# Kernel optimization log

Hardware: AMD Instinct MI355X
Metric: run time of the kernel (lower is better)

Reference implementation:

```python
import jax, jax.numpy as jnp
import numpy as np

ROUTINGS = 3


def squash(v):
    # squash along last axis: v/|v| * |v|^2/(1+|v|^2)
    norm = jnp.linalg.norm(v, axis=-1, keepdims=True)
    ns = norm * norm
    return v / norm * (ns / (1.0 + ns))


def setup_inputs() -> dict:
    key = jax.random.key(0)
    k1, k2 = jax.random.split(key)
    B, N, I, D, Din = 256, 10, 1152, 16, 8
    inputs = jax.random.normal(k1, (B, I, Din), dtype=jnp.float32)
    # glorot-uniform-ish init for W [N, I, D, Din]
    limit = np.sqrt(6.0 / (D + Din)).astype(np.float32)
    W = jax.random.uniform(k2, (N, I, D, Din), dtype=jnp.float32,
                           minval=-limit, maxval=limit)
    return {"inputs": inputs, "W": W}


def reference(inputs, W):
    # inputs: [B, I, Din], W: [N, I, D, Din]
    # u_hat[b,n,i,d] = sum_k W[n,i,d,k] * inputs[b,i,k]  (replaces tf.map_fn)
    u_hat = jnp.einsum('nidk,bik->bnid', W, inputs)  # [B, N, I, D]
    b = jnp.zeros(u_hat.shape[:3], dtype=u_hat.dtype)  # [B, N, I]
    outputs = None
    for r in range(ROUTINGS):
        c = jax.nn.softmax(b, axis=1)  # softmax over output capsules N
        outputs = squash(jnp.einsum('bni,bnid->bnd', c, u_hat))  # [B, N, D]
        if r < ROUTINGS - 1:
            # agreement: a[b,n,i] = <outputs[b,n,:], u_hat[b,n,i,:]>
            b = b + jnp.einsum('bnd,bnid->bni', outputs, u_hat)
    return outputs
```

## Files before the change

### kernel.cpp

```cpp
#include <hip/hip_runtime.h>
#include <hip/hip_bf16.h>
#include <stdint.h>


#define BN 256
#define NN 10
#define II 1152
#define DD 16
#define KK 8
#define NT 18
#define NCH 6
#define CHI 192

typedef unsigned short ushort_t;
typedef unsigned int uint_t;

__device__ __forceinline__ float bflo(uint_t u) {
    union { uint_t i; float f; } v; v.i = u << 16; return v.f;
}
__device__ __forceinline__ float bfhi(uint_t u) {
    union { uint_t i; float f; } v; v.i = u & 0xffff0000u; return v.f;
}
__device__ __forceinline__ uint_t pkbf(float lo, float hi) {
    __hip_bfloat162 h = __float22bfloat162_rn(make_float2(lo, hi));
    uint_t u; __builtin_memcpy(&u, &h, sizeof(u)); return u;
}

__global__ __launch_bounds__(256) void caps_uhat_s0(const float* __restrict__ xg,
                                                    const float* __restrict__ wg,
                                                    ushort_t* __restrict__ u,
                                                    float* __restrict__ part0,
                                                    int b0, int c4)
{
    __shared__ float red[16][NN][16];
    const int tid = threadIdx.x;
    const int lane = tid & 63, wv = tid >> 6;
    const int dq = lane & 3, il = lane >> 2;
    const int nb8 = gridDim.x >> 3;
    const int L   = (blockIdx.x & 7) * nb8 + (blockIdx.x >> 3);
    const int it  = L / c4;
    const int bl  = (L - it * c4) * 4;
    const int i = it * 64 + wv * 16 + il;

    float xv[4][8];
#pragma unroll
    for (int bb = 0; bb < 4; ++bb) {
        const float4* xp = (const float4*)(xg + ((size_t)(b0 + bl + bb) * II + i) * KK);
        float4 x0 = xp[0], x1 = xp[1];
        xv[bb][0] = x0.x; xv[bb][1] = x0.y; xv[bb][2] = x0.z; xv[bb][3] = x0.w;
        xv[bb][4] = x1.x; xv[bb][5] = x1.y; xv[bb][6] = x1.z; xv[bb][7] = x1.w;
    }

    for (int n = 0; n < NN; ++n) {
        const float4* wp = (const float4*)(wg + (size_t)(n * II + i) * (DD * KK)) + dq * 8;
        float4 w[8];
#pragma unroll
        for (int j = 0; j < 8; ++j) w[j] = wp[j];

        float s[4][4];
#pragma unroll
        for (int dj = 0; dj < 4; ++dj) {
            float4 wa = w[2 * dj], wb = w[2 * dj + 1];
#pragma unroll
            for (int bb = 0; bb < 4; ++bb) {
                s[bb][dj] = wa.x * xv[bb][0] + wa.y * xv[bb][1]
                          + wa.z * xv[bb][2] + wa.w * xv[bb][3]
                          + wb.x * xv[bb][4] + wb.y * xv[bb][5]
                          + wb.z * xv[bb][6] + wb.w * xv[bb][7];
            }
        }
#pragma unroll
        for (int bb = 0; bb < 4; ++bb) {
            uint2 q;
            q.x = pkbf(s[bb][0], s[bb][1]);
            q.y = pkbf(s[bb][2], s[bb][3]);
            *(uint2*)(u + (((size_t)(bl + bb) * NN + n) * II + i) * DD + dq * 4) = q;
        }
#pragma unroll
        for (int m = 4; m <= 32; m <<= 1)
#pragma unroll
            for (int bb = 0; bb < 4; ++bb)
#pragma unroll
                for (int dj = 0; dj < 4; ++dj)
                    s[bb][dj] += __shfl_xor(s[bb][dj], m, 64);
        if (il == 0) {
#pragma unroll
            for (int bb = 0; bb < 4; ++bb)
#pragma unroll
                for (int dj = 0; dj < 4; ++dj)
                    red[wv * 4 + dq][n][bb * 4 + dj] = s[bb][dj];
        }
    }
    __syncthreads();
#pragma unroll
    for (int idx = tid; idx < 640; idx += 256) {
        int bb = idx / 160, r = idx - bb * 160;
        int n = r >> 4, d = r & 15, q2 = d >> 2, dj = d & 3;
        float v = red[0 + q2][n][bb * 4 + dj] + red[4 + q2][n][bb * 4 + dj]
                + red[8 + q2][n][bb * 4 + dj] + red[12 + q2][n][bb * 4 + dj];
        part0[((size_t)(b0 + bl + bb) * NT + it) * 160 + r] = 0.1f * v;
    }
}

__device__ __forceinline__ void block_reduce_part(float sp[NN][4], int tid,
                                                  float* red,
                                                  float* __restrict__ partp)
{
#pragma unroll
    for (int m = 4; m <= 32; m <<= 1)
#pragma unroll
        for (int n = 0; n < NN; ++n)
#pragma unroll
            for (int j = 0; j < 4; ++j)
                sp[n][j] += __shfl_xor(sp[n][j], m, 64);

    const int lane = tid & 63, wv = tid >> 6, ld = tid & 3;
    if (lane < 4) {
#pragma unroll
        for (int n = 0; n < NN; ++n)
#pragma unroll
            for (int j = 0; j < 4; ++j)
                red[(wv * NN + n) * 16 + ld * 4 + j] = sp[n][j];
    }
    __syncthreads();
    if (tid < 160) {
        int n = tid >> 4, dd = tid & 15;
        float v = 0.f;
#pragma unroll
        for (int w = 0; w < 4; ++w) v += red[(w * NN + n) * 16 + dd];
        partp[tid] = v;
    }
}

__global__ __launch_bounds__(256) void caps_sweep(const ushort_t* __restrict__ u,
                                                  const float* __restrict__ p0,
                                                  const float* __restrict__ p1,
                                                  float* __restrict__ pout, int b0)
{
    __shared__ float red[4 * 160];
    __shared__ float o_s[160];
    const int tid = threadIdx.x, g = tid >> 2, ld = tid & 3;
    const int cb = blockIdx.x / NCH, ch = blockIdx.x % NCH;
    const int b = b0 + cb;
    const ushort_t* ub = u + (size_t)cb * (NN * II * DD);

    if (tid < 160) {
        float v = 0.f;
#pragma unroll
        for (int t = 0; t < NT; ++t)
            v += p0[((size_t)b * NT + t) * 160 + tid];
        float sq = v * v;
#pragma unroll
        for (int m = 1; m <= 8; m <<= 1) sq += __shfl_xor(sq, m, 64);
        float o = v * (sqrtf(sq) / (1.0f + sq));
        if (p1) {
            float v1 = 0.f;
#pragma unroll
            for (int c2 = 0; c2 < NCH; ++c2)
                v1 += p1[((size_t)b * NCH + c2) * 160 + tid];
            float sq1 = v1 * v1;
#pragma unroll
            for (int m = 1; m <= 8; m <<= 1) sq1 += __shfl_xor(sq1, m, 64);
            o += v1 * (sqrtf(sq1) / (1.0f + sq1));
        }
        o_s[tid] = o;
    }
    __syncthreads();

    float sp[NN][4];
#pragma unroll
    for (int n = 0; n < NN; ++n)
#pragma unroll
        for (int j = 0; j < 4; ++j) sp[n][j] = 0.f;

    const int i0 = ch * CHI + g;
    uint2 r[NN];
#pragma unroll
    for (int n = 0; n < NN; ++n)
        r[n] = *(const uint2*)(ub + ((size_t)(n * II + i0)) * DD + ld * 4);

#pragma unroll
    for (int step = 0; step < CHI / 64; ++step) {
        uint2 rn[NN];
        if (step + 1 < CHI / 64) {
            const int i2 = i0 + (step + 1) * 64;
#pragma unroll
            for (int n = 0; n < NN; ++n)
                rn[n] = *(const uint2*)(ub + ((size_t)(n * II + i2)) * DD + ld * 4);
        }

        float p[NN];
#pragma unroll
        for (int n = 0; n < NN; ++n) {
            float4 o4 = *(const float4*)&o_s[(n << 4) + (ld << 2)];
            p[n] = bflo(r[n].x) * o4.x + bfhi(r[n].x) * o4.y
                 + bflo(r[n].y) * o4.z + bfhi(r[n].y) * o4.w;
        }
        float a[NN];
#pragma unroll
        for (int n = 0; n < NN; ++n) {
            float t2 = p[n] + __shfl_xor(p[n], 1, 64);
            a[n] = t2 + __shfl_xor(t2, 2, 64);
        }
        float m = a[0];
#pragma unroll
        for (int n = 1; n < NN; ++n) m = fmaxf(m, a[n]);
        float c[NN], ssum = 0.f;
#pragma unroll
        for (int n = 0; n < NN; ++n) { c[n] = __expf(a[n] - m); ssum += c[n]; }
        float inv = 1.0f / ssum;
#pragma unroll
        for (int n = 0; n < NN; ++n) {
            float w = c[n] * inv;
            sp[n][0] += w * bflo(r[n].x); sp[n][1] += w * bfhi(r[n].x);
            sp[n][2] += w * bflo(r[n].y); sp[n][3] += w * bfhi(r[n].y);
        }
        if (step + 1 < CHI / 64) {
#pragma unroll
            for (int n = 0; n < NN; ++n) r[n] = rn[n];
        }
    }
    block_reduce_part(sp, tid, red, pout + ((size_t)b * NCH + ch) * 160);
}

__global__ __launch_bounds__(192) void caps_out(const float* __restrict__ p2,
                                                float* __restrict__ out, int b0)
{
    const int b = b0 + blockIdx.x;
    const int t = threadIdx.x;
    if (t < 160) {
        float v = 0.f;
#pragma unroll
        for (int ch = 0; ch < NCH; ++ch)
            v += p2[((size_t)b * NCH + ch) * 160 + t];
        float sq = v * v;
#pragma unroll
        for (int m = 1; m <= 8; m <<= 1) sq += __shfl_xor(sq, m, 64);
        out[(size_t)b * 160 + t] = v * (sqrtf(sq) / (1.0f + sq));
    }
}

extern "C" void kernel_launch(void* const* d_in, const int* in_sizes, int n_in,
                              void* d_out, int out_size, void* d_ws, size_t ws_size,
                              hipStream_t stream)
{
    const float* xg = (const float*)d_in[0];
    const float* wg = (const float*)d_in[1];
    if (n_in >= 2 && in_sizes[0] == NN * II * DD * KK) {
        const float* t = xg; xg = wg; wg = t;
    }
    float* outp = (float*)d_out;

    const size_t perB  = (size_t)NN * II * DD * 2;
    const size_t p0B   = (size_t)BN * NT * 160 * 4;
    const size_t p12B  = (size_t)BN * NCH * 160 * 4;
    size_t extra = p0B + 2 * p12B;
    size_t avail = (ws_size > extra) ? ws_size - extra : 0;
    int C = 256;
    if (avail < (size_t)256 * perB) {
        C = (int)(avail / perB);
        C &= ~15;
        if (C < 16) C = 16;
    }
    ushort_t* uws = (ushort_t*)d_ws;
    float* part0 = (float*)((char*)d_ws + (size_t)C * perB);
    float* part1 = part0 + (size_t)BN * NT * 160;
    float* part2 = part1 + (size_t)BN * NCH * 160;

    for (int b0 = 0; b0 < BN; b0 += C) {
        int c = (BN - b0 < C) ? (BN - b0) : C;
        int c4 = c / 4;
        caps_uhat_s0<<<NT * c4, 256, 0, stream>>>(xg, wg, uws, part0, b0, c4);
        caps_sweep  <<<c * NCH, 256, 0, stream>>>(uws, part0, nullptr, part1, b0);
        caps_sweep  <<<c * NCH, 256, 0, stream>>>(uws, part0, part1,  part2, b0);
        caps_out    <<<c,       192, 0, stream>>>(part2, outp, b0);
    }
}
```

Measured before the change: 168.6 us.

## Use butterfly reduce-scatter in u_hat kernel, halve routing chunks, drop prefetch

The u_hat kernel's 16-value cross-lane sum is replaced with a recursive-halving reduce-scatter. Each shuffle stage now exchanges only half the values, so each lane ends up with one summed value per n, and these are stored into a per-lane shared array. This cuts shuffle count from 64 to 15 per output capsule. Separately, the routing kernels use 3 chunks of 384 capsules instead of 6 of 192, and the manual register double-buffering of u_hat loads is removed. That reduces partial-sum traffic and register pressure, but gives fewer blocks and less explicit latency hiding.

```diff
diff --git a/kernel.cpp b/kernel.cpp
--- a/kernel.cpp
+++ b/kernel.cpp
@@ -9,8 +9,8 @@
 #define DD 16
 #define KK 8
 #define NT 18
-#define NCH 6
-#define CHI 192
+#define NCH 3
+#define CHI 384
 
 typedef unsigned short ushort_t;
 typedef unsigned int uint_t;
@@ -32,7 +32,7 @@
                                                     float* __restrict__ part0,
                                                     int b0, int c4)
 {
-    __shared__ float red[16][NN][16];
+    __shared__ float redn[4][64][NN];
     const int tid = threadIdx.x;
     const int lane = tid & 63, wv = tid >> 6;
     const int dq = lane & 3, il = lane >> 2;
@@ -42,6 +42,9 @@
     const int bl  = (L - it * c4) * 4;
     const int i = it * 64 + wv * 16 + il;
 
+    const bool h0 = (il & 1), h1 = (il >> 1) & 1, h2 = (il >> 2) & 1, h3 = (il >> 3) & 1;
+    float* myred = &redn[wv][lane][0];
+
     float xv[4][8];
 #pragma unroll
     for (int bb = 0; bb < 4; ++bb) {
@@ -76,28 +79,46 @@
             q.y = pkbf(s[bb][2], s[bb][3]);
             *(uint2*)(u + (((size_t)(bl + bb) * NN + n) * II + i) * DD + dq * 4) = q;
         }
-#pragma unroll
-        for (int m = 4; m <= 32; m <<= 1)
-#pragma unroll
-            for (int bb = 0; bb < 4; ++bb)
-#pragma unroll
-                for (int dj = 0; dj < 4; ++dj)
-                    s[bb][dj] += __shfl_xor(s[bb][dj], m, 64);
-        if (il == 0) {
-#pragma unroll
-            for (int bb = 0; bb < 4; ++bb)
-#pragma unroll
-                for (int dj = 0; dj < 4; ++dj)
-                    red[wv * 4 + dq][n][bb * 4 + dj] = s[bb][dj];
+        float v8[8];
+#pragma unroll
+        for (int k = 0; k < 8; ++k) {
+            float a0 = s[(2 * k) >> 2][(2 * k) & 3];
+            float a1 = s[(2 * k + 1) >> 2][(2 * k + 1) & 3];
+            float give = h0 ? a0 : a1;
+            float got  = __shfl_xor(give, 4, 64);
+            v8[k] = (h0 ? a1 : a0) + got;
+        }
+        float v4[4];
+#pragma unroll
+        for (int k = 0; k < 4; ++k) {
+            float a0 = v8[2 * k], a1 = v8[2 * k + 1];
+            float give = h1 ? a0 : a1;
+            float got  = __shfl_xor(give, 8, 64);
+            v4[k] = (h1 ? a1 : a0) + got;
+        }
+        float v2[2];
+#pragma unroll
+        for (int k = 0; k < 2; ++k) {
+            float a0 = v4[2 * k], a1 = v4[2 * k + 1];
+            float give = h2 ? a0 : a1;
+            float got  = __shfl_xor(give, 16, 64);
+            v2[k] = (h2 ? a1 : a0) + got;
+        }
+        {
+            float a0 = v2[0], a1 = v2[1];
+            float give = h3 ? a0 : a1;
+            float got  = __shfl_xor(give, 32, 64);
+            myred[n] = (h3 ? a1 : a0) + got;
         }
     }
     __syncthreads();
 #pragma unroll
     for (int idx = tid; idx < 640; idx += 256) {
         int bb = idx / 160, r = idx - bb * 160;
-        int n = r >> 4, d = r & 15, q2 = d >> 2, dj = d & 3;
-        float v = red[0 + q2][n][bb * 4 + dj] + red[4 + q2][n][bb * 4 + dj]
-                + red[8 + q2][n][bb * 4 + dj] + red[12 + q2][n][bb * 4 + dj];
+        int n = r >> 4, d = r & 15;
+        int lane2 = ((bb * 4 + (d & 3)) << 2) + (d >> 2);
+        float v = redn[0][lane2][n] + redn[1][lane2][n]
+                + redn[2][lane2][n] + redn[3][lane2][n];
         part0[((size_t)(b0 + bl + bb) * NT + it) * 160 + r] = 0.1f * v;
     }
 }
@@ -173,21 +194,12 @@
 #pragma unroll
         for (int j = 0; j < 4; ++j) sp[n][j] = 0.f;
 
-    const int i0 = ch * CHI + g;
-    uint2 r[NN];
-#pragma unroll
-    for (int n = 0; n < NN; ++n)
-        r[n] = *(const uint2*)(ub + ((size_t)(n * II + i0)) * DD + ld * 4);
-
-#pragma unroll
     for (int step = 0; step < CHI / 64; ++step) {
-        uint2 rn[NN];
-        if (step + 1 < CHI / 64) {
-            const int i2 = i0 + (step + 1) * 64;
-#pragma unroll
-            for (int n = 0; n < NN; ++n)
-                rn[n] = *(const uint2*)(ub + ((size_t)(n * II + i2)) * DD + ld * 4);
-        }
+        int i = ch * CHI + step * 64 + g;
+        uint2 r[NN];
+#pragma unroll
+        for (int n = 0; n < NN; ++n)
+            r[n] = *(const uint2*)(ub + ((size_t)(n * II + i)) * DD + ld * 4);
 
         float p[NN];
 #pragma unroll
@@ -214,10 +226,6 @@
             float w = c[n] * inv;
             sp[n][0] += w * bflo(r[n].x); sp[n][1] += w * bfhi(r[n].x);
             sp[n][2] += w * bflo(r[n].y); sp[n][3] += w * bfhi(r[n].y);
-        }
-        if (step + 1 < CHI / 64) {
-#pragma unroll
-            for (int n = 0; n < NN; ++n) r[n] = rn[n];
         }
     }
     block_reduce_part(sp, tid, red, pout + ((size_t)b * NCH + ch) * 160);
```

After: 154.7 us. 8.2% less time.
